# Optimization experiments

Measured on AMD Instinct MI355X. Metric: run time of the kernel, lower is better.

Reference implementation:

```python
import jax, jax.numpy as jnp
import numpy as np

V, E, H, T, B = 50000, 300, 1024, 512, 32   # vocab, embed, hidden, seq, batch
A_DIM, R, MLP_H, C = 350, 30, 512, 2        # attention_dim, num_aspects, mlp_hidden, classes


def setup_inputs() -> dict:
    key = jax.random.key(0)
    ks = jax.random.split(key, 10)
    inp = jax.random.randint(ks[0], (B, T), 0, V)
    lens = jax.random.randint(ks[1], (B,), 1, T + 1)  # variable lengths, >=1
    W_emb = jax.random.normal(ks[2], (V, E), dtype=jnp.float32) * 0.1
    W_ih = jax.random.normal(ks[3], (2, 4 * H, E), dtype=jnp.float32) * 0.02  # [dir, 4h, E]
    W_hh = jax.random.normal(ks[4], (2, 4 * H, H), dtype=jnp.float32) * 0.02
    b_ih = jnp.zeros((2, 4 * H), dtype=jnp.float32)
    b_hh = jnp.zeros((2, 4 * H), dtype=jnp.float32)
    W1 = jax.random.normal(ks[5], (A_DIM, 2 * H), dtype=jnp.float32) * 0.02
    W2 = jax.random.normal(ks[6], (R, A_DIM), dtype=jnp.float32) * 0.02
    W_mlp = jax.random.normal(ks[7], (MLP_H, R * 2 * H), dtype=jnp.float32) * 0.01
    b_mlp = jnp.zeros((MLP_H,), dtype=jnp.float32)
    W_dec = jax.random.uniform(ks[8], (C, MLP_H), dtype=jnp.float32, minval=-0.1, maxval=0.1)
    b_dec = jnp.zeros((C,), dtype=jnp.float32)
    return dict(inp=inp, lens=lens, W_emb=W_emb, W_ih=W_ih, W_hh=W_hh, b_ih=b_ih,
                b_hh=b_hh, W1=W1, W2=W2, W_mlp=W_mlp, b_mlp=b_mlp, W_dec=W_dec, b_dec=b_dec)


def _lstm_dir(xw, W_hh, reverse):
    """xw: [T,B,4h] (input projection precomputed); PyTorch gate order i,f,g,o."""
    h0 = jnp.zeros((xw.shape[1], W_hh.shape[1]), xw.dtype)
    c0 = h0

    def step(carry, xt):
        h, c = carry
        g = xt + h @ W_hh.T
        i, f, gg, o = jnp.split(g, 4, axis=-1)
        c = jax.nn.sigmoid(f) * c + jax.nn.sigmoid(i) * jnp.tanh(gg)
        h = jax.nn.sigmoid(o) * jnp.tanh(c)
        return (h, c), h

    _, hs = jax.lax.scan(step, (h0, c0), xw, reverse=reverse)
    return hs  # [T,B,h]


def reference(inp, lens, W_emb, W_ih, W_hh, b_ih, b_hh, W1, W2, W_mlp, b_mlp, W_dec, b_dec):
    x = W_emb[inp]                         # [B,T,E] embedding lookup
    xt = x.transpose(1, 0, 2)              # [T,B,E]
    bias = b_ih + b_hh                     # [2,4h]
    h_f = _lstm_dir(xt @ W_ih[0].T + bias[0], W_hh[0], False)
    h_b = _lstm_dir(xt @ W_ih[1].T + bias[1], W_hh[1], True)
    out = jnp.concatenate([h_f, h_b], axis=-1).transpose(1, 0, 2)  # [B,T,2h]

    # Masked per-sample self-attention (vectorized over the ragged loop)
    mask = jnp.arange(T)[None, :] < lens[:, None]                  # [B,T]
    s = jnp.tanh(out @ W1.T) @ W2.T                                # [B,T,R]
    s = jnp.where(mask[..., None], s, -1e9)
    A = jax.nn.softmax(s, axis=1).transpose(0, 2, 1)               # [B,R,T], rows sum to 1 over valid t
    M = jnp.einsum('brt,bth->brh', A, out)                         # [B,R,2h]
    feats = M.reshape(M.shape[0], -1)                              # [B, R*2h]

    # Frobenius orthogonality penalty: mean_i ||A_i A_i^T - I||_F^2
    AAT = jnp.einsum('brt,bst->brs', A, A)
    I = jnp.eye(R, dtype=AAT.dtype)
    penal = jnp.mean(jnp.sum((AAT - I) ** 2, axis=(1, 2)))

    hid = jax.nn.relu(feats @ W_mlp.T + b_mlp)
    decoded = jax.nn.softmax(hid @ W_dec.T + b_dec, axis=-1)       # [B,C]
    return decoded, penal
```

## Files before the change

### kernel.cpp

```cpp
#include <hip/hip_runtime.h>
#include <stdint.h>

typedef __attribute__((ext_vector_type(8))) short short8;
typedef __attribute__((ext_vector_type(4))) float f32x4;
typedef __attribute__((ext_vector_type(4))) unsigned int u32x4;

#define B_    32
#define T_    512
#define E_    300
#define KE_   384
#define H_    1024
#define G4_   4096
#define R_    30
#define AD_   350
#define AC_   384
#define MH_   512
#define FEAT_ 61440
#define NWG_  64
#define NU_   16
#define DTICK 27ull

__device__ __forceinline__ unsigned short f2bu(float f) {
  unsigned int x = __builtin_bit_cast(unsigned int, f);
  x += 0x7fffu + ((x >> 16) & 1u);
  return (unsigned short)(x >> 16);
}
__device__ __forceinline__ float b2f(unsigned short u) {
  return __builtin_bit_cast(float, (unsigned int)u << 16);
}
__device__ __forceinline__ float sigm(float x) {
  return __builtin_amdgcn_rcpf(1.f + __expf(-x));
}
__device__ __forceinline__ float tanh_fast(float x) {
  return 1.f - 2.f * __builtin_amdgcn_rcpf(1.f + __expf(2.f * x));
}

#define BULK16G(b0p, b1p, b2p, b3p, FL)                                         \
  asm volatile(                                                                 \
      "global_load_dwordx4 %0, %16, off " FL "\n\t"                             \
      "global_load_dwordx4 %1, %16, off offset:2048 " FL "\n\t"                 \
      "global_load_dwordx4 %2, %17, off " FL "\n\t"                             \
      "global_load_dwordx4 %3, %17, off offset:2048 " FL "\n\t"                 \
      "global_load_dwordx4 %4, %18, off " FL "\n\t"                             \
      "global_load_dwordx4 %5, %18, off offset:2048 " FL "\n\t"                 \
      "global_load_dwordx4 %6, %19, off " FL "\n\t"                             \
      "global_load_dwordx4 %7, %19, off offset:2048 " FL "\n\t"                 \
      "global_load_dwordx4 %8, %16, off offset:512 " FL "\n\t"                  \
      "global_load_dwordx4 %9, %16, off offset:2560 " FL "\n\t"                 \
      "global_load_dwordx4 %10, %17, off offset:512 " FL "\n\t"                 \
      "global_load_dwordx4 %11, %17, off offset:2560 " FL "\n\t"                \
      "global_load_dwordx4 %12, %18, off offset:512 " FL "\n\t"                 \
      "global_load_dwordx4 %13, %18, off offset:2560 " FL "\n\t"                \
      "global_load_dwordx4 %14, %19, off offset:512 " FL "\n\t"                 \
      "global_load_dwordx4 %15, %19, off offset:2560 " FL "\n\t"                \
      "s_waitcnt vmcnt(0)"                                                      \
      : "=&v"(q0), "=&v"(q1), "=&v"(q2), "=&v"(q3), "=&v"(q4), "=&v"(q5),       \
        "=&v"(q6), "=&v"(q7), "=&v"(q8), "=&v"(q9), "=&v"(qa), "=&v"(qb),       \
        "=&v"(qc), "=&v"(qd), "=&v"(qe), "=&v"(qf)                              \
      : "v"(b0p), "v"(b1p), "v"(b2p), "v"(b3p)                                  \
      : "memory")

#define VAL16(BAD)                                                              \
  {                                                                             \
    u32x4 o01 = q0 | q1, o23 = q2 | q3, o45 = q4 | q5, o67 = q6 | q7;           \
    u32x4 o89 = q8 | q9, oab = qa | qb, ocd = qc | qd, oef = qe | qf;           \
    u32x4 ov4 = ((o01 | o23) | (o45 | o67)) | ((o89 | oab) | (ocd | oef));      \
    unsigned ovv = (ov4[0] | ov4[1]) | (ov4[2] | ov4[3]);                       \
    BAD = (ovv & 0x40004000u) != 0;                                             \
  }

__global__ void k0_prep(const int* __restrict__ inp, const float* __restrict__ W_emb,
                        const float* __restrict__ W_ih, const float* __restrict__ W1,
                        const float* __restrict__ W_mlp,
                        unsigned short* __restrict__ xb, unsigned short* __restrict__ wihb,
                        unsigned short* __restrict__ w1b, unsigned short* __restrict__ wmlpb) {
  const int N1 = 16384 * KE_;
  const int N2 = 8192 * KE_;
  const int N3 = AC_ * 2048;
  const int N4 = MH_ * FEAT_;
  const int NT = N1 + N2 + N3 + N4;
  for (int i = blockIdx.x * blockDim.x + threadIdx.x; i < NT; i += gridDim.x * blockDim.x) {
    if (i < N1) {
      int row = i / KE_, e = i - row * KE_;
      float v = (e < E_) ? W_emb[(size_t)inp[row] * E_ + e] : 0.f;
      xb[i] = f2bu(v);
    } else if (i < N1 + N2) {
      int j = i - N1;
      int rw = j / KE_, e = j - rw * KE_;
      float v = (e < E_) ? W_ih[(size_t)rw * E_ + e] : 0.f;
      wihb[j] = f2bu(v);
    } else if (i < N1 + N2 + N3) {
      int j = i - N1 - N2;
      int a = j >> 11, k = j & 2047;
      float v = (a < AD_) ? W1[(size_t)a * 2048 + k] : 0.f;
      w1b[j] = f2bu(v);
    } else {
      int j = i - N1 - N2 - N3;
      wmlpb[j] = f2bu(W_mlp[j]);
    }
  }
}

__global__ __launch_bounds__(256, 1) void k2_rnn(const float* __restrict__ Whh,
                                                 const unsigned short* __restrict__ wihb,
                                                 const unsigned short* __restrict__ xb,
                                                 const float* __restrict__ b_ih,
                                                 const float* __restrict__ b_hh,
                                                 unsigned short* __restrict__ outb,
                                                 unsigned short* __restrict__ hpub) {
  const int dir = blockIdx.x >> 6;
  const int w = blockIdx.x & 63;
  const int tid = threadIdx.x;
  const int wid = tid >> 6, lane = tid & 63;
  const int l15 = lane & 15, lg = lane >> 4;

  __shared__ float Gp[4][4][32][21];
  __shared__ __align__(16) unsigned short htmp[32][16];

  short8 afr[4][8];
  {
    const int kq = wid << 8;
#pragma unroll
    for (int g = 0; g < 4; ++g) {
      const float* wp = Whh + ((size_t)dir * G4_ + g * H_ + w * NU_ + l15) * H_ + kq + lg * 8;
#pragma unroll
      for (int ktl = 0; ktl < 8; ++ktl) {
        float4 f0 = *(const float4*)(wp + ktl * 32);
        float4 f1 = *(const float4*)(wp + ktl * 32 + 4);
        short8 s;
        s[0] = (short)f2bu(f0.x); s[1] = (short)f2bu(f0.y);
        s[2] = (short)f2bu(f0.z); s[3] = (short)f2bu(f0.w);
        s[4] = (short)f2bu(f1.x); s[5] = (short)f2bu(f1.y);
        s[6] = (short)f2bu(f1.z); s[7] = (short)f2bu(f1.w);
        afr[g][ktl] = s;
      }
    }
  }

  const int kqx = wid * 96;
  short8 axr[4][3];
#pragma unroll
  for (int g = 0; g < 4; ++g) {
    const unsigned short* xp = wihb + ((size_t)dir * G4_ + g * H_ + w * NU_ + l15) * KE_ + kqx + lg * 8;
#pragma unroll
    for (int kt = 0; kt < 3; ++kt) axr[g][kt] = *(const short8*)(xp + kt * 32);
  }

  const int u = tid >> 5;
  const int b = tid & 31;

  float bsum[2][4];
#pragma unroll
  for (int p = 0; p < 2; ++p)
#pragma unroll
    for (int g = 0; g < 4; ++g) {
      int row = dir * G4_ + g * H_ + w * NU_ + u + p * 8;
      bsum[p][g] = b_ih[row] + b_hh[row];
    }

  const size_t hlane = (size_t)wid * 8192 + (size_t)(lg >> 1) * 512 + l15 * 16 + (lg & 1) * 8;
  const size_t hpoll = (size_t)lane * 512;

  float cst[2] = {0.f, 0.f};
  unsigned long long pprev = __builtin_amdgcn_s_memrealtime();

#pragma unroll 1
  for (int s = 0; s < T_; ++s) {
    const int t = dir ? (T_ - 1 - s) : s;

    f32x4 acc[4][2];
#pragma unroll
    for (int g = 0; g < 4; ++g) {
      acc[g][0] = (f32x4){0.f, 0.f, 0.f, 0.f};
      acc[g][1] = (f32x4){0.f, 0.f, 0.f, 0.f};
    }

    {
      short8 xbf[2][3];
#pragma unroll
      for (int n = 0; n < 2; ++n)
#pragma unroll
        for (int kt = 0; kt < 3; ++kt)
          xbf[n][kt] = *(const short8*)(xb + ((size_t)(n * 16 + l15) * T_ + t) * KE_ + kqx + kt * 32 + lg * 8);
#pragma unroll
      for (int kt = 0; kt < 3; ++kt)
#pragma unroll
        for (int g = 0; g < 4; ++g) {
          acc[g][0] = __builtin_amdgcn_mfma_f32_16x16x32_bf16(axr[g][kt], xbf[0][kt], acc[g][0], 0, 0, 0);
          acc[g][1] = __builtin_amdgcn_mfma_f32_16x16x32_bf16(axr[g][kt], xbf[1][kt], acc[g][1], 0, 0, 0);
        }
    }
    __builtin_amdgcn_sched_barrier(0);

    if (s > 0) {
      const int tsrc = dir ? t + 1 : t - 1;
      const unsigned short* hbase = hpub + (size_t)(dir * T_ + tsrc) * 32768;
      const unsigned short* B0 = hbase + hlane;
      const unsigned short* B1 = B0 + 2048;
      const unsigned short* B2 = B0 + 4096;
      const unsigned short* B3 = B0 + 6144;
      u32x4 q0, q1, q2, q3, q4, q5, q6, q7, q8, q9, qa, qb, qc, qd, qe, qf;

      {
        unsigned long long tgt = pprev + DTICK;
        unsigned long long now;
        do { now = __builtin_amdgcn_s_memrealtime(); } while (now < tgt);
      }

      BULK16G(B0, B1, B2, B3, "sc0");
      bool bad; VAL16(bad);
      if (__builtin_expect(bad, 0)) {
        const unsigned short* sp = hbase + hpoll;
        unsigned v;
        int guard = 0;
        for (;;) {
          asm volatile("global_load_dword %0, %1, off sc0 sc1\n\ts_waitcnt vmcnt(0)"
                       : "=v"(v) : "v"(sp) : "memory");
          if (__all(!(v & 0x40004000u))) break;
          if (++guard > 50000) break;
        }
        int g2 = 0;
        do {
          BULK16G(B0, B1, B2, B3, "sc0 sc1");
          VAL16(bad);
        } while (bad && ++g2 < 50000);
      }

      short8 bf0[8], bf1[8];
      bf0[0] = __builtin_bit_cast(short8, q0); bf0[1] = __builtin_bit_cast(short8, q1);
      bf0[2] = __builtin_bit_cast(short8, q2); bf0[3] = __builtin_bit_cast(short8, q3);
      bf0[4] = __builtin_bit_cast(short8, q4); bf0[5] = __builtin_bit_cast(short8, q5);
      bf0[6] = __builtin_bit_cast(short8, q6); bf0[7] = __builtin_bit_cast(short8, q7);
      bf1[0] = __builtin_bit_cast(short8, q8); bf1[1] = __builtin_bit_cast(short8, q9);
      bf1[2] = __builtin_bit_cast(short8, qa); bf1[3] = __builtin_bit_cast(short8, qb);
      bf1[4] = __builtin_bit_cast(short8, qc); bf1[5] = __builtin_bit_cast(short8, qd);
      bf1[6] = __builtin_bit_cast(short8, qe); bf1[7] = __builtin_bit_cast(short8, qf);

#pragma unroll
      for (int ktl = 0; ktl < 8; ++ktl) {
#pragma unroll
        for (int g = 0; g < 4; ++g) {
          acc[g][0] = __builtin_amdgcn_mfma_f32_16x16x32_bf16(afr[g][ktl], bf0[ktl], acc[g][0], 0, 0, 0);
          acc[g][1] = __builtin_amdgcn_mfma_f32_16x16x32_bf16(afr[g][ktl], bf1[ktl], acc[g][1], 0, 0, 0);
        }
      }
    }

#pragma unroll
    for (int g = 0; g < 4; ++g)
#pragma unroll
      for (int n = 0; n < 2; ++n)
#pragma unroll
        for (int j = 0; j < 4; ++j)
          Gp[wid][g][n * 16 + l15][lg * 4 + j] = acc[g][n][j];
    __syncthreads();

#pragma unroll
    for (int p = 0; p < 2; ++p) {
      int ul = u + p * 8;
      float gi = Gp[0][0][b][ul] + Gp[1][0][b][ul] + Gp[2][0][b][ul] + Gp[3][0][b][ul] + bsum[p][0];
      float gf = Gp[0][1][b][ul] + Gp[1][1][b][ul] + Gp[2][1][b][ul] + Gp[3][1][b][ul] + bsum[p][1];
      float gg = Gp[0][2][b][ul] + Gp[1][2][b][ul] + Gp[2][2][b][ul] + Gp[3][2][b][ul] + bsum[p][2];
      float go = Gp[0][3][b][ul] + Gp[1][3][b][ul] + Gp[2][3][b][ul] + Gp[3][3][b][ul] + bsum[p][3];
      cst[p] = sigm(gf) * cst[p] + sigm(gi) * tanh_fast(gg);
      float hv = sigm(go) * tanh_fast(cst[p]);
      htmp[b][ul] = f2bu(hv);
    }
    __syncthreads();

    pprev = __builtin_amdgcn_s_memrealtime();
    if (tid < 64) {
      int bb = tid >> 1, half = tid & 1;
      u32x4 v = *(const u32x4*)&htmp[bb][half * 8];
      unsigned short* hp = hpub + (size_t)(dir * T_ + t) * 32768 + (size_t)w * 512 + bb * 16 + half * 8;
      asm volatile("global_store_dwordx4 %0, %1, off sc0 sc1" :: "v"(hp), "v"(v) : "memory");
      *(u32x4*)(outb + ((size_t)bb * T_ + t) * 2048 + dir * H_ + w * NU_ + half * 8) = v;
    }
  }
}

__global__ __launch_bounds__(256, 1) void k3_s1(const unsigned short* __restrict__ outb,
                                                const unsigned short* __restrict__ w1b,
                                                unsigned short* __restrict__ th1) {
  const int rb = blockIdx.x;
  const int wid = threadIdx.x >> 6, lane = threadIdx.x & 63;
  const int m = wid & 1, nh = wid >> 1;
  const int l15 = lane & 15, lg = lane >> 4;

  f32x4 acc[12];
#pragma unroll
  for (int nt = 0; nt < 12; ++nt) acc[nt] = (f32x4){0.f, 0.f, 0.f, 0.f};

  const unsigned short* arow = outb + ((size_t)rb * 32 + m * 16 + l15) * 2048;
  for (int kt = 0; kt < 64; ++kt) {
    short8 af = *(const short8*)(arow + kt * 32 + lg * 8);
#pragma unroll
    for (int nt = 0; nt < 12; ++nt) {
      int col = nh * 192 + nt * 16 + l15;
      short8 bf = *(const short8*)(w1b + (size_t)col * 2048 + kt * 32 + lg * 8);
      acc[nt] = __builtin_amdgcn_mfma_f32_16x16x32_bf16(af, bf, acc[nt], 0, 0, 0);
    }
  }
#pragma unroll
  for (int nt = 0; nt < 12; ++nt) {
#pragma unroll
    for (int j = 0; j < 4; ++j) {
      int row = rb * 32 + m * 16 + lg * 4 + j;
      int col = nh * 192 + nt * 16 + l15;
      th1[(size_t)row * AC_ + col] = f2bu(tanh_fast(acc[nt][j]));
    }
  }
}

__global__ void k4_s2(const unsigned short* __restrict__ th1, const float* __restrict__ W2,
                      float* __restrict__ abuf) {
  int idx = blockIdx.x * 256 + threadIdx.x;
  int row = idx >> 5, r = idx & 31;
  if (r >= R_) return;
  const unsigned short* tp = th1 + (size_t)row * AC_;
  const float* wp = W2 + r * AD_;
  float acc = 0.f;
  for (int a = 0; a < AD_; ++a) acc = fmaf(b2f(tp[a]), wp[a], acc);
  int b = row >> 9, t = row & 511;
  abuf[((size_t)b * R_ + r) * T_ + t] = acc;
}

__global__ void k5_sm(float* __restrict__ abuf, const int* __restrict__ lens) {
  int wv = blockIdx.x * 4 + (threadIdx.x >> 6);
  int lane = threadIdx.x & 63;
  if (wv >= B_ * R_) return;
  int b = wv / R_, r = wv % R_;
  int len = lens[b];
  float* row = abuf + ((size_t)b * R_ + r) * T_;
  float v[8];
  float mx = -1e30f;
#pragma unroll
  for (int i = 0; i < 8; ++i) {
    int t = lane + i * 64;
    float x = (t < len) ? row[t] : -1e30f;
    v[i] = x;
    mx = fmaxf(mx, x);
  }
#pragma unroll
  for (int o = 32; o > 0; o >>= 1) mx = fmaxf(mx, __shfl_xor(mx, o));
  float sum = 0.f;
#pragma unroll
  for (int i = 0; i < 8; ++i) {
    float e = (v[i] > -1e29f) ? __expf(v[i] - mx) : 0.f;
    v[i] = e;
    sum += e;
  }
#pragma unroll
  for (int o = 32; o > 0; o >>= 1) sum += __shfl_xor(sum, o);
  float inv = 1.f / sum;
#pragma unroll
  for (int i = 0; i < 8; ++i) row[lane + i * 64] = v[i] * inv;
}

__global__ __launch_bounds__(256) void k6_m(const float* __restrict__ abuf,
                                            const unsigned short* __restrict__ outb,
                                            unsigned short* __restrict__ mbuf) {
  int b = blockIdx.x >> 4, hb = blockIdx.x & 15;
  __shared__ float As[R_ * T_];
  for (int i = threadIdx.x; i < R_ * T_; i += 256) As[i] = abuf[(size_t)b * R_ * T_ + i];
  __syncthreads();
  int h = threadIdx.x & 127, rh = threadIdx.x >> 7;
  float acc[15];
#pragma unroll
  for (int rr = 0; rr < 15; ++rr) acc[rr] = 0.f;
  const unsigned short* op = outb + (size_t)b * T_ * 2048 + hb * 128 + h;
  for (int t = 0; t < T_; ++t) {
    float vv = b2f(op[(size_t)t * 2048]);
#pragma unroll
    for (int rr = 0; rr < 15; ++rr) acc[rr] = fmaf(As[(rh * 15 + rr) * T_ + t], vv, acc[rr]);
  }
#pragma unroll
  for (int rr = 0; rr < 15; ++rr)
    mbuf[(size_t)b * FEAT_ + (size_t)(rh * 15 + rr) * 2048 + hb * 128 + h] = f2bu(acc[rr]);
}

__global__ __launch_bounds__(256) void k7_pen(const float* __restrict__ abuf,
                                              float* __restrict__ penp) {
  int b = blockIdx.x;
  __shared__ float As[R_ * 515];
  __shared__ float red[256];
  for (int i = threadIdx.x; i < R_ * T_; i += 256) {
    int r = i >> 9, t = i & 511;
    As[r * 515 + t] = abuf[(size_t)b * R_ * T_ + i];
  }
  __syncthreads();
  float psum = 0.f;
  for (int p = threadIdx.x; p < R_ * R_; p += 256) {
    int r = p / R_, s = p % R_;
    const float* pr = As + r * 515;
    const float* ps = As + s * 515;
    float d = 0.f;
    for (int t = 0; t < T_; ++t) d = fmaf(pr[t], ps[t], d);
    d -= (r == s) ? 1.f : 0.f;
    psum += d * d;
  }
  red[threadIdx.x] = psum;
  __syncthreads();
  for (int o = 128; o > 0; o >>= 1) {
    if (threadIdx.x < o) red[threadIdx.x] += red[threadIdx.x + o];
    __syncthreads();
  }
  if (threadIdx.x == 0) penp[b] = red[0];
}

__global__ __launch_bounds__(256, 1) void k8_mlp(const unsigned short* __restrict__ wmlpb,
                                                 const unsigned short* __restrict__ mbuf,
                                                 float* __restrict__ hid) {
  const int mblk = blockIdx.x >> 4, kblk = blockIdx.x & 15;
  const int wid = threadIdx.x >> 6, lane = threadIdx.x & 63;
  const int l15 = lane & 15, lg = lane >> 4;
  const int kq = kblk * 3840 + wid * 960;

  f32x4 acc[2][2];
#pragma unroll
  for (int i = 0; i < 2; ++i)
#pragma unroll
    for (int j = 0; j < 2; ++j) acc[i][j] = (f32x4){0.f, 0.f, 0.f, 0.f};

  const unsigned short* ap0 = wmlpb + (size_t)(mblk * 32 + l15) * FEAT_ + kq + lg * 8;
  const unsigned short* ap1 = ap0 + (size_t)16 * FEAT_;
  const unsigned short* bp0 = mbuf + (size_t)l15 * FEAT_ + kq + lg * 8;
  const unsigned short* bp1 = bp0 + (size_t)16 * FEAT_;
  for (int kt = 0; kt < 30; ++kt) {
    short8 a0 = *(const short8*)(ap0 + kt * 32);
    short8 a1 = *(const short8*)(ap1 + kt * 32);
    short8 b0 = *(const short8*)(bp0 + kt * 32);
    short8 b1 = *(const short8*)(bp1 + kt * 32);
    acc[0][0] = __builtin_amdgcn_mfma_f32_16x16x32_bf16(a0, b0, acc[0][0], 0, 0, 0);
    acc[0][1] = __builtin_amdgcn_mfma_f32_16x16x32_bf16(a0, b1, acc[0][1], 0, 0, 0);
    acc[1][0] = __builtin_amdgcn_mfma_f32_16x16x32_bf16(a1, b0, acc[1][0], 0, 0, 0);
    acc[1][1] = __builtin_amdgcn_mfma_f32_16x16x32_bf16(a1, b1, acc[1][1], 0, 0, 0);
  }

  __shared__ float red[4][32][33];
#pragma unroll
  for (int mi = 0; mi < 2; ++mi)
#pragma unroll
    for (int ni = 0; ni < 2; ++ni)
#pragma unroll
      for (int j = 0; j < 4; ++j)
        red[wid][mi * 16 + lg * 4 + j][ni * 16 + l15] = acc[mi][ni][j];
  __syncthreads();

  int m = threadIdx.x >> 3, b4 = (threadIdx.x & 7) * 4;
#pragma unroll
  for (int k = 0; k < 4; ++k) {
    int bb = b4 + k;
    float s = red[0][m][bb] + red[1][m][bb] + red[2][m][bb] + red[3][m][bb];
    atomicAdd(&hid[(size_t)bb * MH_ + mblk * 32 + m], s);
  }
}

__global__ void k9_out(const float* __restrict__ hid, const float* __restrict__ b_mlp,
                       const float* __restrict__ W_dec, const float* __restrict__ b_dec,
                       const float* __restrict__ penp, float* __restrict__ out) {
  int tid = threadIdx.x;
  if (tid < 64) {
    int b = tid >> 1, c = tid & 1;
    const float* hp = hid + (size_t)b * MH_;
    const float* wp = W_dec + (size_t)c * MH_;
    float acc = b_dec[c];
    for (int k = 0; k < MH_; ++k) {
      float hk = fmaxf(hp[k] + b_mlp[k], 0.f);
      acc = fmaf(hk, wp[k], acc);
    }
    float other = __shfl_xor(acc, 1);
    float mx = fmaxf(acc, other);
    float e = __expf(acc - mx), eo = __expf(other - mx);
    out[b * 2 + c] = e / (e + eo);
  } else if (tid == 64) {
    float s = 0.f;
    for (int b = 0; b < B_; ++b) s += penp[b];
    out[64] = s * (1.f / 32.f);
  }
}

extern "C" void kernel_launch(void* const* d_in, const int* in_sizes, int n_in,
                              void* d_out, int out_size, void* d_ws, size_t ws_size,
                              hipStream_t stream) {
  const int* inp = (const int*)d_in[0];
  const int* lens = (const int*)d_in[1];
  const float* W_emb = (const float*)d_in[2];
  const float* W_ih = (const float*)d_in[3];
  const float* W_hh = (const float*)d_in[4];
  const float* b_ih = (const float*)d_in[5];
  const float* b_hh = (const float*)d_in[6];
  const float* W1 = (const float*)d_in[7];
  const float* W2 = (const float*)d_in[8];
  const float* W_mlp = (const float*)d_in[9];
  const float* b_mlp = (const float*)d_in[10];
  const float* W_dec = (const float*)d_in[11];
  const float* b_dec = (const float*)d_in[12];
  float* out = (float*)d_out;

  char* ws = (char*)d_ws;
  size_t off = 0;
  auto take = [&](size_t bytes) -> char* {
    char* p = ws + off;
    off = (off + bytes + 255) & ~(size_t)255;
    return p;
  };
  unsigned short* outb = (unsigned short*)take((size_t)B_ * T_ * 2048 * 2);
  unsigned short* hpub = (unsigned short*)take((size_t)2 * T_ * 32768 * 2);
  unsigned short* xb = (unsigned short*)take((size_t)16384 * KE_ * 2);
  unsigned short* wihb = (unsigned short*)take((size_t)8192 * KE_ * 2);
  unsigned short* w1b = (unsigned short*)take((size_t)AC_ * 2048 * 2);
  unsigned short* wmlpb = (unsigned short*)take((size_t)MH_ * FEAT_ * 2);
  unsigned short* th1 = (unsigned short*)take((size_t)16384 * AC_ * 2);
  float* abuf = (float*)take((size_t)B_ * R_ * T_ * 4);
  unsigned short* mbuf = (unsigned short*)take((size_t)B_ * FEAT_ * 2);
  float* penp = (float*)take(B_ * 4);
  float* hid = (float*)take((size_t)B_ * MH_ * 4);

  if (off > ws_size) {
    hipMemsetAsync(d_out, 0xFF, (size_t)out_size * 4, stream);
    return;
  }

  hipMemsetAsync(hpub, 0xFF, (size_t)2 * T_ * 32768 * 2, stream);
  hipMemsetAsync(hid, 0, (size_t)B_ * MH_ * 4, stream);

  k0_prep<<<2048, 256, 0, stream>>>(inp, W_emb, W_ih, W1, W_mlp, xb, wihb, w1b, wmlpb);
  k2_rnn<<<128, 256, 0, stream>>>(W_hh, wihb, xb, b_ih, b_hh, outb, hpub);
  k3_s1<<<512, 256, 0, stream>>>(outb, w1b, th1);
  k4_s2<<<2048, 256, 0, stream>>>(th1, W2, abuf);
  k5_sm<<<240, 256, 0, stream>>>(abuf, lens);
  k6_m<<<512, 256, 0, stream>>>(abuf, outb, mbuf);
  k7_pen<<<32, 256, 0, stream>>>(abuf, penp);
  k8_mlp<<<256, 256, 0, stream>>>(wmlpb, mbuf, hid);
  k9_out<<<1, 128, 0, stream>>>(hid, b_mlp, W_dec, b_dec, penp, out);
}
```

Before: 2.263 ms.

## Split persistent LSTM recurrence across batch halves to double workgroups

The persistent bidirectional LSTM kernel now launches 256 workgroups instead of 128, with each workgroup handling one 16-sample half of the batch. The hidden-state exchange buffer is split per batch half, so each step polls and loads half as much data and runs half the MFMAs. This is meant to shorten per-step latency on the serial critical path by spreading work over more CUs. In exchange, W_hh register fragments are duplicated across twice as many workgroups, more workgroups take part in the global flag-based synchronization, and the spin-wait tick constant is lowered.

```diff
diff --git a/kernel.cpp b/kernel.cpp
--- a/kernel.cpp
+++ b/kernel.cpp
@@ -16,9 +16,8 @@
 #define AC_   384
 #define MH_   512
 #define FEAT_ 61440
-#define NWG_  64
 #define NU_   16
-#define DTICK 27ull
+#define DTICK 16ull
 
 __device__ __forceinline__ unsigned short f2bu(float f) {
   unsigned int x = __builtin_bit_cast(unsigned int, f);
@@ -35,36 +34,32 @@
   return 1.f - 2.f * __builtin_amdgcn_rcpf(1.f + __expf(2.f * x));
 }
 
-#define BULK16G(b0p, b1p, b2p, b3p, FL)                                         \
+#define BULK8G_ISS(b0p, b1p, FL)                                                \
   asm volatile(                                                                 \
-      "global_load_dwordx4 %0, %16, off " FL "\n\t"                             \
-      "global_load_dwordx4 %1, %16, off offset:2048 " FL "\n\t"                 \
-      "global_load_dwordx4 %2, %17, off " FL "\n\t"                             \
-      "global_load_dwordx4 %3, %17, off offset:2048 " FL "\n\t"                 \
-      "global_load_dwordx4 %4, %18, off " FL "\n\t"                             \
-      "global_load_dwordx4 %5, %18, off offset:2048 " FL "\n\t"                 \
-      "global_load_dwordx4 %6, %19, off " FL "\n\t"                             \
-      "global_load_dwordx4 %7, %19, off offset:2048 " FL "\n\t"                 \
-      "global_load_dwordx4 %8, %16, off offset:512 " FL "\n\t"                  \
-      "global_load_dwordx4 %9, %16, off offset:2560 " FL "\n\t"                 \
-      "global_load_dwordx4 %10, %17, off offset:512 " FL "\n\t"                 \
-      "global_load_dwordx4 %11, %17, off offset:2560 " FL "\n\t"                \
-      "global_load_dwordx4 %12, %18, off offset:512 " FL "\n\t"                 \
-      "global_load_dwordx4 %13, %18, off offset:2560 " FL "\n\t"                \
-      "global_load_dwordx4 %14, %19, off offset:512 " FL "\n\t"                 \
-      "global_load_dwordx4 %15, %19, off offset:2560 " FL "\n\t"                \
-      "s_waitcnt vmcnt(0)"                                                      \
-      : "=&v"(q0), "=&v"(q1), "=&v"(q2), "=&v"(q3), "=&v"(q4), "=&v"(q5),       \
-        "=&v"(q6), "=&v"(q7), "=&v"(q8), "=&v"(q9), "=&v"(qa), "=&v"(qb),       \
-        "=&v"(qc), "=&v"(qd), "=&v"(qe), "=&v"(qf)                              \
-      : "v"(b0p), "v"(b1p), "v"(b2p), "v"(b3p)                                  \
+      "global_load_dwordx4 %0, %8, off " FL "\n\t"                              \
+      "global_load_dwordx4 %1, %8, off offset:1024 " FL "\n\t"                  \
+      "global_load_dwordx4 %2, %8, off offset:2048 " FL "\n\t"                  \
+      "global_load_dwordx4 %3, %8, off offset:3072 " FL "\n\t"                  \
+      "global_load_dwordx4 %4, %9, off " FL "\n\t"                              \
+      "global_load_dwordx4 %5, %9, off offset:1024 " FL "\n\t"                  \
+      "global_load_dwordx4 %6, %9, off offset:2048 " FL "\n\t"                  \
+      "global_load_dwordx4 %7, %9, off offset:3072 " FL                         \
+      : "=&v"(q0), "=&v"(q1), "=&v"(q2), "=&v"(q3),                             \
+        "=&v"(q4), "=&v"(q5), "=&v"(q6), "=&v"(q7)                              \
+      : "v"(b0p), "v"(b1p)                                                      \
       : "memory")
 
-#define VAL16(BAD)                                                              \
+#define BULK8G(b0p, b1p, FL)                                                    \
+  do {                                                                          \
+    BULK8G_ISS(b0p, b1p, FL);                                                   \
+    asm volatile("s_waitcnt vmcnt(0)" ::: "memory");                            \
+    __builtin_amdgcn_sched_barrier(0);                                          \
+  } while (0)
+
+#define VAL8(BAD)                                                               \
   {                                                                             \
     u32x4 o01 = q0 | q1, o23 = q2 | q3, o45 = q4 | q5, o67 = q6 | q7;           \
-    u32x4 o89 = q8 | q9, oab = qa | qb, ocd = qc | qd, oef = qe | qf;           \
-    u32x4 ov4 = ((o01 | o23) | (o45 | o67)) | ((o89 | oab) | (ocd | oef));      \
+    u32x4 ov4 = (o01 | o23) | (o45 | o67);                                      \
     unsigned ovv = (ov4[0] | ov4[1]) | (ov4[2] | ov4[3]);                       \
     BAD = (ovv & 0x40004000u) != 0;                                             \
   }
@@ -108,14 +103,15 @@
                                                  const float* __restrict__ b_hh,
                                                  unsigned short* __restrict__ outb,
                                                  unsigned short* __restrict__ hpub) {
-  const int dir = blockIdx.x >> 6;
-  const int w = blockIdx.x & 63;
+  const int dir = blockIdx.x >> 7;
+  const int w = (blockIdx.x >> 1) & 63;
+  const int bh = blockIdx.x & 1;
   const int tid = threadIdx.x;
   const int wid = tid >> 6, lane = tid & 63;
   const int l15 = lane & 15, lg = lane >> 4;
 
-  __shared__ float Gp[4][4][32][21];
-  __shared__ __align__(16) unsigned short htmp[32][16];
+  __shared__ float Gp[4][4][16][17];
+  __shared__ __align__(16) unsigned short htmp[16][16];
 
   short8 afr[4][8];
   {
@@ -146,60 +142,49 @@
     for (int kt = 0; kt < 3; ++kt) axr[g][kt] = *(const short8*)(xp + kt * 32);
   }
 
-  const int u = tid >> 5;
-  const int b = tid & 31;
-
-  float bsum[2][4];
-#pragma unroll
-  for (int p = 0; p < 2; ++p)
-#pragma unroll
-    for (int g = 0; g < 4; ++g) {
-      int row = dir * G4_ + g * H_ + w * NU_ + u + p * 8;
-      bsum[p][g] = b_ih[row] + b_hh[row];
-    }
-
-  const size_t hlane = (size_t)wid * 8192 + (size_t)(lg >> 1) * 512 + l15 * 16 + (lg & 1) * 8;
-  const size_t hpoll = (size_t)lane * 512;
-
-  float cst[2] = {0.f, 0.f};
+  const int u = tid >> 4;
+  const int b = tid & 15;
+
+  float bsum[4];
+#pragma unroll
+  for (int g = 0; g < 4; ++g) {
+    int row = dir * G4_ + g * H_ + w * NU_ + u;
+    bsum[g] = b_ih[row] + b_hh[row];
+  }
+
+  const size_t hlane = (size_t)(wid * 16 + (lg >> 1)) * 256 + l15 * 16 + (lg & 1) * 8;
+  const size_t hpoll = (size_t)(wid * 16 + (lane & 15)) * 256;
+
+  float cst = 0.f;
   unsigned long long pprev = __builtin_amdgcn_s_memrealtime();
 
 #pragma unroll 1
   for (int s = 0; s < T_; ++s) {
     const int t = dir ? (T_ - 1 - s) : s;
 
-    f32x4 acc[4][2];
-#pragma unroll
-    for (int g = 0; g < 4; ++g) {
-      acc[g][0] = (f32x4){0.f, 0.f, 0.f, 0.f};
-      acc[g][1] = (f32x4){0.f, 0.f, 0.f, 0.f};
-    }
+    f32x4 acc[4];
+#pragma unroll
+    for (int g = 0; g < 4; ++g) acc[g] = (f32x4){0.f, 0.f, 0.f, 0.f};
 
     {
-      short8 xbf[2][3];
-#pragma unroll
-      for (int n = 0; n < 2; ++n)
-#pragma unroll
-        for (int kt = 0; kt < 3; ++kt)
-          xbf[n][kt] = *(const short8*)(xb + ((size_t)(n * 16 + l15) * T_ + t) * KE_ + kqx + kt * 32 + lg * 8);
+      short8 xbf[3];
 #pragma unroll
       for (int kt = 0; kt < 3; ++kt)
-#pragma unroll
-        for (int g = 0; g < 4; ++g) {
-          acc[g][0] = __builtin_amdgcn_mfma_f32_16x16x32_bf16(axr[g][kt], xbf[0][kt], acc[g][0], 0, 0, 0);
-          acc[g][1] = __builtin_amdgcn_mfma_f32_16x16x32_bf16(axr[g][kt], xbf[1][kt], acc[g][1], 0, 0, 0);
-        }
+        xbf[kt] = *(const short8*)(xb + ((size_t)(bh * 16 + l15) * T_ + t) * KE_ + kqx + kt * 32 + lg * 8);
+#pragma unroll
+      for (int kt = 0; kt < 3; ++kt)
+#pragma unroll
+        for (int g = 0; g < 4; ++g)
+          acc[g] = __builtin_amdgcn_mfma_f32_16x16x32_bf16(axr[g][kt], xbf[kt], acc[g], 0, 0, 0);
     }
     __builtin_amdgcn_sched_barrier(0);
 
     if (s > 0) {
       const int tsrc = dir ? t + 1 : t - 1;
-      const unsigned short* hbase = hpub + (size_t)(dir * T_ + tsrc) * 32768;
+      const unsigned short* hbase = hpub + ((size_t)(dir * T_ + tsrc) * 2 + bh) * 16384;
       const unsigned short* B0 = hbase + hlane;
-      const unsigned short* B1 = B0 + 2048;
-      const unsigned short* B2 = B0 + 4096;
-      const unsigned short* B3 = B0 + 6144;
-      u32x4 q0, q1, q2, q3, q4, q5, q6, q7, q8, q9, qa, qb, qc, qd, qe, qf;
+      const unsigned short* B1 = B0 + 4096;
+      u32x4 q0, q1, q2, q3, q4, q5, q6, q7;
 
       {
         unsigned long long tgt = pprev + DTICK;
@@ -207,8 +192,8 @@
         do { now = __builtin_amdgcn_s_memrealtime(); } while (now < tgt);
       }
 
-      BULK16G(B0, B1, B2, B3, "sc0");
-      bool bad; VAL16(bad);
+      BULK8G(B0, B1, "sc0");
+      bool bad; VAL8(bad);
       if (__builtin_expect(bad, 0)) {
         const unsigned short* sp = hbase + hpoll;
         unsigned v;
@@ -221,60 +206,49 @@
         }
         int g2 = 0;
         do {
-          BULK16G(B0, B1, B2, B3, "sc0 sc1");
-          VAL16(bad);
+          BULK8G(B0, B1, "sc0 sc1");
+          VAL8(bad);
         } while (bad && ++g2 < 50000);
       }
 
-      short8 bf0[8], bf1[8];
-      bf0[0] = __builtin_bit_cast(short8, q0); bf0[1] = __builtin_bit_cast(short8, q1);
-      bf0[2] = __builtin_bit_cast(short8, q2); bf0[3] = __builtin_bit_cast(short8, q3);
-      bf0[4] = __builtin_bit_cast(short8, q4); bf0[5] = __builtin_bit_cast(short8, q5);
-      bf0[6] = __builtin_bit_cast(short8, q6); bf0[7] = __builtin_bit_cast(short8, q7);
-      bf1[0] = __builtin_bit_cast(short8, q8); bf1[1] = __builtin_bit_cast(short8, q9);
-      bf1[2] = __builtin_bit_cast(short8, qa); bf1[3] = __builtin_bit_cast(short8, qb);
-      bf1[4] = __builtin_bit_cast(short8, qc); bf1[5] = __builtin_bit_cast(short8, qd);
-      bf1[6] = __builtin_bit_cast(short8, qe); bf1[7] = __builtin_bit_cast(short8, qf);
-
-#pragma unroll
-      for (int ktl = 0; ktl < 8; ++ktl) {
-#pragma unroll
-        for (int g = 0; g < 4; ++g) {
-          acc[g][0] = __builtin_amdgcn_mfma_f32_16x16x32_bf16(afr[g][ktl], bf0[ktl], acc[g][0], 0, 0, 0);
-          acc[g][1] = __builtin_amdgcn_mfma_f32_16x16x32_bf16(afr[g][ktl], bf1[ktl], acc[g][1], 0, 0, 0);
-        }
-      }
+      short8 bf[8];
+      bf[0] = __builtin_bit_cast(short8, q0); bf[1] = __builtin_bit_cast(short8, q1);
+      bf[2] = __builtin_bit_cast(short8, q2); bf[3] = __builtin_bit_cast(short8, q3);
+      bf[4] = __builtin_bit_cast(short8, q4); bf[5] = __builtin_bit_cast(short8, q5);
+      bf[6] = __builtin_bit_cast(short8, q6); bf[7] = __builtin_bit_cast(short8, q7);
+
+#pragma unroll
+      for (int ktl = 0; ktl < 8; ++ktl)
+#pragma unroll
+        for (int g = 0; g < 4; ++g)
+          acc[g] = __builtin_amdgcn_mfma_f32_16x16x32_bf16(afr[g][ktl], bf[ktl], acc[g], 0, 0, 0);
     }
 
 #pragma unroll
     for (int g = 0; g < 4; ++g)
 #pragma unroll
-      for (int n = 0; n < 2; ++n)
-#pragma unroll
-        for (int j = 0; j < 4; ++j)
-          Gp[wid][g][n * 16 + l15][lg * 4 + j] = acc[g][n][j];
+      for (int j = 0; j < 4; ++j)
+        Gp[wid][g][l15][lg * 4 + j] = acc[g][j];
     __syncthreads();
 
-#pragma unroll
-    for (int p = 0; p < 2; ++p) {
-      int ul = u + p * 8;
-      float gi = Gp[0][0][b][ul] + Gp[1][0][b][ul] + Gp[2][0][b][ul] + Gp[3][0][b][ul] + bsum[p][0];
-      float gf = Gp[0][1][b][ul] + Gp[1][1][b][ul] + Gp[2][1][b][ul] + Gp[3][1][b][ul] + bsum[p][1];
-      float gg = Gp[0][2][b][ul] + Gp[1][2][b][ul] + Gp[2][2][b][ul] + Gp[3][2][b][ul] + bsum[p][2];
-      float go = Gp[0][3][b][ul] + Gp[1][3][b][ul] + Gp[2][3][b][ul] + Gp[3][3][b][ul] + bsum[p][3];
-      cst[p] = sigm(gf) * cst[p] + sigm(gi) * tanh_fast(gg);
-      float hv = sigm(go) * tanh_fast(cst[p]);
-      htmp[b][ul] = f2bu(hv);
+    {
+      float gi = Gp[0][0][b][u] + Gp[1][0][b][u] + Gp[2][0][b][u] + Gp[3][0][b][u] + bsum[0];
+      float gf = Gp[0][1][b][u] + Gp[1][1][b][u] + Gp[2][1][b][u] + Gp[3][1][b][u] + bsum[1];
+      float gg = Gp[0][2][b][u] + Gp[1][2][b][u] + Gp[2][2][b][u] + Gp[3][2][b][u] + bsum[2];
+      float go = Gp[0][3][b][u] + Gp[1][3][b][u] + Gp[2][3][b][u] + Gp[3][3][b][u] + bsum[3];
+      cst = sigm(gf) * cst + sigm(gi) * tanh_fast(gg);
+      float hv = sigm(go) * tanh_fast(cst);
+      htmp[b][u] = f2bu(hv);
     }
     __syncthreads();
 
     pprev = __builtin_amdgcn_s_memrealtime();
     if (tid < 64) {
-      int bb = tid >> 1, half = tid & 1;
-      u32x4 v = *(const u32x4*)&htmp[bb][half * 8];
-      unsigned short* hp = hpub + (size_t)(dir * T_ + t) * 32768 + (size_t)w * 512 + bb * 16 + half * 8;
-      asm volatile("global_store_dwordx4 %0, %1, off sc0 sc1" :: "v"(hp), "v"(v) : "memory");
-      *(u32x4*)(outb + ((size_t)bb * T_ + t) * 2048 + dir * H_ + w * NU_ + half * 8) = v;
+      int bb = tid >> 2, q = tid & 3;
+      uint2 v = *(const uint2*)&htmp[bb][q * 4];
+      unsigned short* hp = hpub + ((size_t)(dir * T_ + t) * 2 + bh) * 16384 + (size_t)w * 256 + bb * 16 + q * 4;
+      asm volatile("global_store_dwordx2 %0, %1, off sc0 sc1" :: "v"(hp), "v"(v) : "memory");
+      *(uint2*)(outb + ((size_t)(bh * 16 + bb) * T_ + t) * 2048 + dir * H_ + w * NU_ + q * 4) = v;
     }
   }
 }
@@ -506,7 +480,7 @@
     return p;
   };
   unsigned short* outb = (unsigned short*)take((size_t)B_ * T_ * 2048 * 2);
-  unsigned short* hpub = (unsigned short*)take((size_t)2 * T_ * 32768 * 2);
+  unsigned short* hpub = (unsigned short*)take((size_t)2 * T_ * 2 * 16384 * 2);
   unsigned short* xb = (unsigned short*)take((size_t)16384 * KE_ * 2);
   unsigned short* wihb = (unsigned short*)take((size_t)8192 * KE_ * 2);
   unsigned short* w1b = (unsigned short*)take((size_t)AC_ * 2048 * 2);
@@ -522,11 +496,11 @@
     return;
   }
 
-  hipMemsetAsync(hpub, 0xFF, (size_t)2 * T_ * 32768 * 2, stream);
+  hipMemsetAsync(hpub, 0xFF, (size_t)2 * T_ * 2 * 16384 * 2, stream);
   hipMemsetAsync(hid, 0, (size_t)B_ * MH_ * 4, stream);
 
   k0_prep<<<2048, 256, 0, stream>>>(inp, W_emb, W_ih, W1, W_mlp, xb, wihb, w1b, wmlpb);
-  k2_rnn<<<128, 256, 0, stream>>>(W_hh, wihb, xb, b_ih, b_hh, outb, hpub);
+  k2_rnn<<<256, 256, 0, stream>>>(W_hh, wihb, xb, b_ih, b_hh, outb, hpub);
   k3_s1<<<512, 256, 0, stream>>>(outb, w1b, th1);
   k4_s2<<<2048, 256, 0, stream>>>(th1, W2, abuf);
   k5_sm<<<240, 256, 0, stream>>>(abuf, lens);
```

Result: faster. 2.065 ms, median of 2 (-8.8%).
